# Kernel tuning notes

Measured on AMD Instinct MI355X. Metric: run time of the kernel, lower is better.

Reference implementation:

```python
import jax, jax.numpy as jnp
import numpy as np

B, N, S, F = 16, 512, 7, 256
HID, NUM_CLASSES = 1024, 81
FLAT = S * S * F  # 12544


def setup_inputs() -> dict:
    key = jax.random.key(0)
    ks = jax.random.split(key, 8)
    features = jax.random.normal(ks[0], (B, N, S, S, F), dtype=jnp.float32)
    valid_mask = jax.random.randint(ks[1], (B, N), 0, 2) > 0
    W1 = jax.random.normal(ks[2], (FLAT, HID), dtype=jnp.float32) * (1.0 / np.sqrt(FLAT))
    b1 = jnp.zeros((HID,), dtype=jnp.float32)
    W2 = jax.random.normal(ks[3], (HID, HID), dtype=jnp.float32) * (1.0 / np.sqrt(HID))
    b2 = jnp.zeros((HID,), dtype=jnp.float32)
    W3 = jax.random.normal(ks[4], (HID, NUM_CLASSES), dtype=jnp.float32) * (1.0 / np.sqrt(HID))
    b3 = jnp.zeros((NUM_CLASSES,), dtype=jnp.float32)
    return {"features": features, "valid_mask": valid_mask, "W1": W1, "b1": b1,
            "W2": W2, "b2": b2, "W3": W3, "b3": b3, "features_size_pred": N}


def reference(features, valid_mask, W1, b1, W2, b2, W3, b3, features_size_pred):
    # The TF module masks out invalid ROIs, runs the MLP, then scatters results
    # back to original positions (pad + argsort + gather) with zeros for invalid
    # rows. That is mathematically identical to running the MLP on all ROIs and
    # zeroing invalid rows, which is the efficient dense form.
    b, n = features.shape[0], features.shape[1]
    x = features.reshape(b * n, FLAT)                      # [B*N, 12544]
    h = jax.nn.relu(x @ W1 + b1)                           # [B*N, HID]
    h = jax.nn.relu(h @ W2 + b2)                           # [B*N, HID]
    logits = (h @ W3 + b3).reshape(b, n, NUM_CLASSES)      # [B, N, C]
    mask = valid_mask.astype(logits.dtype)[..., None]      # [B, N, 1]
    return logits * mask
```

## Files before the change

### kernel.cpp

```cpp
#include <hip/hip_runtime.h>
#include <stdint.h>

#define DEVINL __device__ __forceinline__

typedef __bf16 bf16x8 __attribute__((ext_vector_type(8)));
typedef float f32x4 __attribute__((ext_vector_type(4)));

DEVINL unsigned short f32_to_bf16(float f) {
  union { float f; uint32_t u; } v;
  v.f = f;
  uint32_t r = v.u + 0x7fffu + ((v.u >> 16) & 1u);
  return (unsigned short)(r >> 16);
}

DEVINL void load16_to_lds(const void* g, void* l) {
  __builtin_amdgcn_global_load_lds(
      (const __attribute__((address_space(1))) void*)g,
      (__attribute__((address_space(3))) void*)l, 16, 0, 0);
}

__global__ __launch_bounds__(256) void cast_f32_bf16_kernel(
    const float* __restrict__ in, unsigned short* __restrict__ out) {
  size_t idx = (size_t)blockIdx.x * 256 + threadIdx.x;
  const float4* in4 = (const float4*)in;
  float4 a = in4[2 * idx];
  float4 b = in4[2 * idx + 1];
  uint4 p;
  p.x = (uint32_t)f32_to_bf16(a.x) | ((uint32_t)f32_to_bf16(a.y) << 16);
  p.y = (uint32_t)f32_to_bf16(a.z) | ((uint32_t)f32_to_bf16(a.w) << 16);
  p.z = (uint32_t)f32_to_bf16(b.x) | ((uint32_t)f32_to_bf16(b.y) << 16);
  p.w = (uint32_t)f32_to_bf16(b.z) | ((uint32_t)f32_to_bf16(b.w) << 16);
  reinterpret_cast<uint4*>(out)[idx] = p;
}

__global__ void transpose_cast_kernel(const float* __restrict__ W,
                                      unsigned short* __restrict__ Wt,
                                      int K, int Nsrc) {
  __shared__ float tile[32][33];
  const int k0 = blockIdx.x * 32;
  const int n0 = blockIdx.y * 32;
  const int t = threadIdx.x;
#pragma unroll
  for (int i = 0; i < 4; ++i) {
    int idx = t + 256 * i;
    int r = idx >> 5, c = idx & 31;
    int gn = n0 + c;
    float v = (gn < Nsrc) ? W[(size_t)(k0 + r) * Nsrc + gn] : 0.0f;
    tile[r][c] = v;
  }
  __syncthreads();
#pragma unroll
  for (int i = 0; i < 4; ++i) {
    int idx = t + 256 * i;
    int n = idx >> 5, k = idx & 31;
    Wt[(size_t)(n0 + n) * K + (k0 + k)] = f32_to_bf16(tile[k][n]);
  }
}

template <int BM, int BN, bool A_F32, bool RELU_BF16_OUT>
__global__ __launch_bounds__(256) void gemm_kernel(
    const void* __restrict__ Ap, const unsigned short* __restrict__ Bt,
    const float* __restrict__ bias, unsigned short* __restrict__ Hout,
    float* __restrict__ Fout, const int* __restrict__ mask, int K, int Nout,
    int ldo) {
  constexpr int WM = BM / 32;
  constexpr int WN = BN / 32;
  __shared__ alignas(16) unsigned short Asmem[BM * 32];
  __shared__ alignas(16) unsigned short Bsmem[BN * 32];

  const int tid = threadIdx.x;
  const int wave = tid >> 6, lane = tid & 63;
  const int wm = wave >> 1, wn = wave & 1;
  const int m0 = blockIdx.y * BM;
  const int n0 = blockIdx.x * BN;

  const float* Af = (const float*)Ap;
  const unsigned short* Ab = (const unsigned short*)Ap;

  f32x4 acc[WM][WN] = {};

  for (int k0 = 0; k0 < K; k0 += 32) {
    if constexpr (A_F32) {
      constexpr int NF4 = (BM * 32) / (256 * 4);
#pragma unroll
      for (int i = 0; i < NF4; ++i) {
        int idx = tid + 256 * i;
        int r = idx >> 3, c4 = idx & 7;
        float4 v = *reinterpret_cast<const float4*>(
            Af + (size_t)(m0 + r) * K + (k0 + c4 * 4));
        uint2 p;
        p.x = (uint32_t)f32_to_bf16(v.x) | ((uint32_t)f32_to_bf16(v.y) << 16);
        p.y = (uint32_t)f32_to_bf16(v.z) | ((uint32_t)f32_to_bf16(v.w) << 16);
        *reinterpret_cast<uint2*>(&Asmem[r * 32 + c4 * 4]) = p;
      }
    } else {
#pragma unroll
      for (int c = wave; c < BM / 16; c += 4) {
        int row = c * 16 + (lane >> 2);
        load16_to_lds(Ab + (size_t)(m0 + row) * K + (k0 + (lane & 3) * 8),
                      &Asmem[c * 512]);
      }
    }
#pragma unroll
    for (int c = wave; c < BN / 16; c += 4) {
      int row = c * 16 + (lane >> 2);
      load16_to_lds(Bt + (size_t)(n0 + row) * K + (k0 + (lane & 3) * 8),
                    &Bsmem[c * 512]);
    }
    __syncthreads();

    bf16x8 a[WM], b[WN];
#pragma unroll
    for (int i = 0; i < WM; ++i)
      a[i] = *reinterpret_cast<const bf16x8*>(
          &Asmem[(wm * WM * 16 + i * 16 + (lane & 15)) * 32 + (lane >> 4) * 8]);
#pragma unroll
    for (int j = 0; j < WN; ++j)
      b[j] = *reinterpret_cast<const bf16x8*>(
          &Bsmem[(wn * WN * 16 + j * 16 + (lane & 15)) * 32 + (lane >> 4) * 8]);
#pragma unroll
    for (int i = 0; i < WM; ++i)
#pragma unroll
      for (int j = 0; j < WN; ++j)
        acc[i][j] = __builtin_amdgcn_mfma_f32_16x16x32_bf16(a[i], b[j],
                                                            acc[i][j], 0, 0, 0);
    __syncthreads();
  }

  const int l15 = lane & 15, quad = lane >> 4;
#pragma unroll
  for (int j = 0; j < WN; ++j) {
    int n = n0 + wn * WN * 16 + j * 16 + l15;
    if (n >= Nout) continue;
    float bn = bias[n];
#pragma unroll
    for (int i = 0; i < WM; ++i) {
      int mb = m0 + wm * WM * 16 + i * 16 + quad * 4;
      f32x4 v = acc[i][j];
#pragma unroll
      for (int r = 0; r < 4; ++r) {
        int m = mb + r;
        if constexpr (RELU_BF16_OUT) {
          Hout[(size_t)m * ldo + n] = f32_to_bf16(fmaxf(v[r] + bn, 0.0f));
        } else {
          Fout[(size_t)m * ldo + n] = (v[r] + bn) * (mask[m] ? 1.0f : 0.0f);
        }
      }
    }
  }
}

extern "C" void kernel_launch(void* const* d_in, const int* in_sizes, int n_in,
                              void* d_out, int out_size, void* d_ws,
                              size_t ws_size, hipStream_t stream) {
  const float* feat = (const float*)d_in[0];
  const int* mask = (const int*)d_in[1];
  const float* W1 = (const float*)d_in[2];
  const float* b1 = (const float*)d_in[3];
  const float* W2 = (const float*)d_in[4];
  const float* b2 = (const float*)d_in[5];
  const float* W3 = (const float*)d_in[6];
  const float* b3 = (const float*)d_in[7];
  float* out = (float*)d_out;

  char* ws = (char*)d_ws;
  size_t off = 0;
  unsigned short* W1t = (unsigned short*)(ws + off); off += 25690112;
  unsigned short* W2t = (unsigned short*)(ws + off); off += 2097152;
  unsigned short* W3t = (unsigned short*)(ws + off); off += 196608;
  unsigned short* H1  = (unsigned short*)(ws + off); off += 16777216;
  unsigned short* H2  = (unsigned short*)(ws + off); off += 16777216;
  unsigned short* Fb  = (unsigned short*)(ws + off);
  size_t need = off + 205520896;

  transpose_cast_kernel<<<dim3(392, 32), 256, 0, stream>>>(W1, W1t, 12544, 1024);
  transpose_cast_kernel<<<dim3(32, 32), 256, 0, stream>>>(W2, W2t, 1024, 1024);
  transpose_cast_kernel<<<dim3(32, 3), 256, 0, stream>>>(W3, W3t, 1024, 81);

  if (ws_size >= need) {
    cast_f32_bf16_kernel<<<50176, 256, 0, stream>>>(feat, Fb);
    gemm_kernel<128, 128, false, true><<<dim3(8, 64), 256, 0, stream>>>(
        Fb, W1t, b1, H1, nullptr, nullptr, 12544, 1024, 1024);
  } else {
    gemm_kernel<128, 128, true, true><<<dim3(8, 64), 256, 0, stream>>>(
        feat, W1t, b1, H1, nullptr, nullptr, 12544, 1024, 1024);
  }
  gemm_kernel<128, 128, false, true><<<dim3(8, 64), 256, 0, stream>>>(
      H1, W2t, b2, H2, nullptr, nullptr, 1024, 1024, 1024);
  gemm_kernel<32, 96, false, false><<<dim3(1, 256), 256, 0, stream>>>(
      H2, W3t, b3, nullptr, out, mask, 1024, 81, 81);
}
```

Baseline: 998.6 us.

## Compact valid ROIs and run the MLP only on masked-in rows

Adds a single-block prefix-scan kernel that builds a compacted index list of valid ROIs and a count. The feature gather/cast and all three GEMMs then process only the valid rows (padded to 128), and blocks beyond the padded count exit early. The output is pre-zeroed and the final GEMM scatters results back to the original row positions. With about half the mask set this roughly halves GEMM and cast work, at the cost of an extra serial scan kernel, a zero-fill pass, and indirect row addressing.

```diff
diff --git a/kernel.cpp b/kernel.cpp
--- a/kernel.cpp
+++ b/kernel.cpp
@@ -19,18 +19,63 @@
       (__attribute__((address_space(3))) void*)l, 16, 0, 0);
 }
 
-__global__ __launch_bounds__(256) void cast_f32_bf16_kernel(
-    const float* __restrict__ in, unsigned short* __restrict__ out) {
-  size_t idx = (size_t)blockIdx.x * 256 + threadIdx.x;
-  const float4* in4 = (const float4*)in;
-  float4 a = in4[2 * idx];
-  float4 b = in4[2 * idx + 1];
+__global__ __launch_bounds__(1024) void compact_kernel(
+    const int* __restrict__ mask, int* __restrict__ ridx, int* __restrict__ nv) {
+  __shared__ int tsum[1024];
+  __shared__ int wbase[17];
+  const int t = threadIdx.x;
+  int flags[8];
+  int cnt = 0;
+#pragma unroll
+  for (int i = 0; i < 8; ++i) {
+    flags[i] = (mask[t * 8 + i] != 0) ? 1 : 0;
+    cnt += flags[i];
+  }
+  tsum[t] = cnt;
+  __syncthreads();
+  if ((t & 63) == 0) {
+    int s = 0;
+    for (int i = 0; i < 64; ++i) { int v = tsum[t + i]; tsum[t + i] = s; s += v; }
+    wbase[t >> 6] = s;
+  }
+  __syncthreads();
+  if (t == 0) {
+    int s = 0;
+    for (int w = 0; w < 16; ++w) { int v = wbase[w]; wbase[w] = s; s += v; }
+    wbase[16] = s;
+    *nv = s;
+  }
+  __syncthreads();
+  int base = wbase[t >> 6] + tsum[t];
+#pragma unroll
+  for (int i = 0; i < 8; ++i)
+    if (flags[i]) ridx[base++] = t * 8 + i;
+  const int Mv = wbase[16];
+  const int Mpad = (Mv + 127) & ~127;
+  for (int i = Mv + t; i < Mpad; i += 1024) ridx[i] = 0;
+}
+
+__global__ __launch_bounds__(256) void zero_out_kernel(float4* __restrict__ o) {
+  o[(size_t)blockIdx.x * 256 + threadIdx.x] = float4{0.f, 0.f, 0.f, 0.f};
+}
+
+__global__ __launch_bounds__(256) void gather_cast_kernel(
+    const float* __restrict__ feat, const int* __restrict__ ridx,
+    const int* __restrict__ nv, unsigned short* __restrict__ out) {
+  const int Mpad = ((*nv) + 127) & ~127;
+  const unsigned idx = blockIdx.x * 256u + threadIdx.x;
+  const unsigned crow = idx / 1568u;
+  if ((int)crow >= Mpad) return;
+  const int off = (int)(idx - crow * 1568u) * 8;
+  const float* src = feat + (size_t)ridx[crow] * 12544 + off;
+  float4 a = *reinterpret_cast<const float4*>(src);
+  float4 b = *reinterpret_cast<const float4*>(src + 4);
   uint4 p;
   p.x = (uint32_t)f32_to_bf16(a.x) | ((uint32_t)f32_to_bf16(a.y) << 16);
   p.y = (uint32_t)f32_to_bf16(a.z) | ((uint32_t)f32_to_bf16(a.w) << 16);
   p.z = (uint32_t)f32_to_bf16(b.x) | ((uint32_t)f32_to_bf16(b.y) << 16);
   p.w = (uint32_t)f32_to_bf16(b.z) | ((uint32_t)f32_to_bf16(b.w) << 16);
-  reinterpret_cast<uint4*>(out)[idx] = p;
+  *reinterpret_cast<uint4*>(out + (size_t)crow * 12544 + off) = p;
 }
 
 __global__ void transpose_cast_kernel(const float* __restrict__ W,
@@ -61,17 +106,21 @@
 __global__ __launch_bounds__(256) void gemm_kernel(
     const void* __restrict__ Ap, const unsigned short* __restrict__ Bt,
     const float* __restrict__ bias, unsigned short* __restrict__ Hout,
-    float* __restrict__ Fout, const int* __restrict__ mask, int K, int Nout,
-    int ldo) {
+    float* __restrict__ Fout, const int* __restrict__ ridx,
+    const int* __restrict__ nv, int K, int Nout, int ldo) {
   constexpr int WM = BM / 32;
   constexpr int WN = BN / 32;
+  const int Mv = *nv;
+  const int Mpad = (Mv + 127) & ~127;
+  const int m0 = blockIdx.y * BM;
+  if (m0 >= Mpad) return;
+
   __shared__ alignas(16) unsigned short Asmem[BM * 32];
   __shared__ alignas(16) unsigned short Bsmem[BN * 32];
 
   const int tid = threadIdx.x;
   const int wave = tid >> 6, lane = tid & 63;
   const int wm = wave >> 1, wn = wave & 1;
-  const int m0 = blockIdx.y * BM;
   const int n0 = blockIdx.x * BN;
 
   const float* Af = (const float*)Ap;
@@ -87,7 +136,7 @@
         int idx = tid + 256 * i;
         int r = idx >> 3, c4 = idx & 7;
         float4 v = *reinterpret_cast<const float4*>(
-            Af + (size_t)(m0 + r) * K + (k0 + c4 * 4));
+            Af + (size_t)ridx[m0 + r] * K + (k0 + c4 * 4));
         uint2 p;
         p.x = (uint32_t)f32_to_bf16(v.x) | ((uint32_t)f32_to_bf16(v.y) << 16);
         p.y = (uint32_t)f32_to_bf16(v.z) | ((uint32_t)f32_to_bf16(v.w) << 16);
@@ -143,7 +192,7 @@
         if constexpr (RELU_BF16_OUT) {
           Hout[(size_t)m * ldo + n] = f32_to_bf16(fmaxf(v[r] + bn, 0.0f));
         } else {
-          Fout[(size_t)m * ldo + n] = (v[r] + bn) * (mask[m] ? 1.0f : 0.0f);
+          if (m < Mv) Fout[(size_t)ridx[m] * ldo + n] = v[r] + bn;
         }
       }
     }
@@ -165,6 +214,8 @@
 
   char* ws = (char*)d_ws;
   size_t off = 0;
+  int* ridx = (int*)(ws + off); off += 32768;
+  int* nv   = (int*)(ws + off); off += 256;
   unsigned short* W1t = (unsigned short*)(ws + off); off += 25690112;
   unsigned short* W2t = (unsigned short*)(ws + off); off += 2097152;
   unsigned short* W3t = (unsigned short*)(ws + off); off += 196608;
@@ -173,20 +224,22 @@
   unsigned short* Fb  = (unsigned short*)(ws + off);
   size_t need = off + 205520896;
 
+  compact_kernel<<<1, 1024, 0, stream>>>(mask, ridx, nv);
+  zero_out_kernel<<<648, 256, 0, stream>>>((float4*)out);
   transpose_cast_kernel<<<dim3(392, 32), 256, 0, stream>>>(W1, W1t, 12544, 1024);
   transpose_cast_kernel<<<dim3(32, 32), 256, 0, stream>>>(W2, W2t, 1024, 1024);
   transpose_cast_kernel<<<dim3(32, 3), 256, 0, stream>>>(W3, W3t, 1024, 81);
 
   if (ws_size >= need) {
-    cast_f32_bf16_kernel<<<50176, 256, 0, stream>>>(feat, Fb);
+    gather_cast_kernel<<<50176, 256, 0, stream>>>(feat, ridx, nv, Fb);
     gemm_kernel<128, 128, false, true><<<dim3(8, 64), 256, 0, stream>>>(
-        Fb, W1t, b1, H1, nullptr, nullptr, 12544, 1024, 1024);
+        Fb, W1t, b1, H1, nullptr, ridx, nv, 12544, 1024, 1024);
   } else {
     gemm_kernel<128, 128, true, true><<<dim3(8, 64), 256, 0, stream>>>(
-        feat, W1t, b1, H1, nullptr, nullptr, 12544, 1024, 1024);
+        feat, W1t, b1, H1, nullptr, ridx, nv, 12544, 1024, 1024);
   }
   gemm_kernel<128, 128, false, true><<<dim3(8, 64), 256, 0, stream>>>(
-      H1, W2t, b2, H2, nullptr, nullptr, 1024, 1024, 1024);
+      H1, W2t, b2, H2, nullptr, ridx, nv, 1024, 1024, 1024);
   gemm_kernel<32, 96, false, false><<<dim3(1, 256), 256, 0, stream>>>(
-      H2, W3t, b3, nullptr, out, mask, 1024, 81, 81);
-}
+      H2, W3t, b3, nullptr, out, ridx, nv, 1024, 81, 81);
+}
```

Result: faster. 964.0 us (-3.5%).
